# Kernel tuning notes

Measured on AMD Instinct MI355X. Metric: run time of the kernel, lower is better.

Reference implementation:

```python
import jax, jax.numpy as jnp
import numpy as np

L, D, H, FF, I, MAXREL = 6, 512, 8, 2048, 50, 128
HD = D // H
NREL = 2 * MAXREL + 1
EPS = 1e-5


def setup_inputs() -> dict:
    key = jax.random.key(0)
    ks = jax.random.split(key, 32)
    s = 0.02
    p = {
        'x': jax.random.normal(ks[0], (16, 512, I), dtype=jnp.float32),
        'in_w': jax.random.normal(ks[1], (I, D)) * s,
        'in_b': jnp.zeros((D,), jnp.float32),
        'Wq': jax.random.normal(ks[2], (L, D, D)) * s,
        'Wk': jax.random.normal(ks[3], (L, D, D)) * s,
        'Wv': jax.random.normal(ks[4], (L, D, D)) * s,
        'Wo': jax.random.normal(ks[5], (L, D, D)) * s,
        'bo': jnp.zeros((L, D), jnp.float32),
        'rel_emb': jax.random.normal(ks[6], (L, NREL, HD)) * s,
        'w1': jax.random.normal(ks[7], (L, D, FF)) * s,
        'b1': jnp.zeros((L, FF), jnp.float32),
        'w2': jax.random.normal(ks[8], (L, FF, D)) * s,
        'b2': jnp.zeros((L, D), jnp.float32),
        'ln1_g': jnp.ones((L, D), jnp.float32),
        'ln1_b': jnp.zeros((L, D), jnp.float32),
        'ln2_g': jnp.ones((L, D), jnp.float32),
        'ln2_b': jnp.zeros((L, D), jnp.float32),
        'on_g': jnp.ones((D,), jnp.float32),
        'on_b': jnp.zeros((D,), jnp.float32),
        'p1_w': jax.random.normal(ks[9], (D, D // 2)) * s,
        'p1_b': jnp.zeros((D // 2,), jnp.float32),
        'p2_w': jax.random.normal(ks[10], (D // 2, 1)) * s,
        'p2_b': jnp.zeros((1,), jnp.float32),
    }
    return p


def _layer_norm(x, g, b):
    m = jnp.mean(x, axis=-1, keepdims=True)
    v = jnp.mean(jnp.square(x - m), axis=-1, keepdims=True)
    return (x - m) * jax.lax.rsqrt(v + EPS) * g + b


def _sinusoidal_pe(seq_len, d_model):
    pos = jnp.arange(seq_len, dtype=jnp.float32)[:, None]
    div = jnp.exp(jnp.arange(0, d_model, 2, dtype=jnp.float32) * (-jnp.log(10000.0) / d_model))
    pe = jnp.zeros((seq_len, d_model), jnp.float32)
    pe = pe.at[:, 0::2].set(jnp.sin(pos * div))
    pe = pe.at[:, 1::2].set(jnp.cos(pos * div))
    return pe


def reference(x, in_w, in_b, Wq, Wk, Wv, Wo, bo, rel_emb, w1, b1, w2, b2,
              ln1_g, ln1_b, ln2_g, ln2_b, on_g, on_b, p1_w, p1_b, p2_w, p2_b):
    B, S, _ = x.shape
    scale = jnp.sqrt(jnp.float32(HD))
    # relative position index matrix [S, S] in [0, 2*MAXREL]
    r = jnp.arange(S)
    rel_idx = jnp.clip(r[None, :] - r[:, None], -MAXREL, MAXREL) + MAXREL

    h = x @ in_w + in_b                       # [B,S,D]
    h = h + _sinusoidal_pe(S, D)

    for l in range(L):
        q = (h @ Wq[l]).reshape(B, S, H, HD).transpose(0, 2, 1, 3)  # [B,H,S,hd]
        k = (h @ Wk[l]).reshape(B, S, H, HD).transpose(0, 2, 1, 3)
        v = (h @ Wv[l]).reshape(B, S, H, HD).transpose(0, 2, 1, 3)
        scores = jnp.einsum('bhqd,bhkd->bhqk', q, k) / scale
        rel = rel_emb[l][rel_idx]             # [S,S,hd]
        scores = scores + jnp.einsum('bhqd,qkd->bhqk', q, rel)  # rel bias is NOT scaled (matches source)
        attn = jax.nn.softmax(scores, axis=-1)
        ctx = jnp.einsum('bhqk,bhkd->bhqd', attn, v)
        ctx = ctx.transpose(0, 2, 1, 3).reshape(B, S, D)
        attn_out = ctx @ Wo[l] + bo[l]
        h = _layer_norm(h + attn_out, ln1_g[l], ln1_b[l])
        ff = jax.nn.relu(h @ w1[l] + b1[l]) @ w2[l] + b2[l]
        h = _layer_norm(h + ff, ln2_g[l], ln2_b[l])

    h = _layer_norm(h, on_g, on_b)
    out = jax.nn.relu(h @ p1_w + p1_b) @ p2_w + p2_b  # [B,S,1]
    return out
```

## Files before the change

### kernel.cpp

```cpp
#include <hip/hip_runtime.h>

typedef unsigned short u16;
typedef unsigned int   u32;
typedef short   short8  __attribute__((ext_vector_type(8)));
typedef float   floatx4 __attribute__((ext_vector_type(4)));
typedef int     intx4   __attribute__((ext_vector_type(4)));

#define NTOK 8192
#define SEQ  512
#define NLAYER 6

#define OFF_WT   ((size_t)0)
#define OFF_HB   ((size_t)38010880)
#define OFF_QKV  ((size_t)46399488)
#define OFF_CTX  ((size_t)71565312)
#define OFF_GOUT ((size_t)79953920)
#define OFF_FF   ((size_t)96731136)
#define OFF_HD1  ((size_t)130285568)
#define OFF_VT   OFF_FF
#define OFF_RELB OFF_HD1

#define LSTRIDE 3145728
#define P1T_OFF 18874368

__device__ __forceinline__ float b2f(u16 v) { return __uint_as_float(((u32)v) << 16); }
__device__ __forceinline__ float lo16(u32 v) { return __uint_as_float(v << 16); }
__device__ __forceinline__ float hi16(u32 v) { return __uint_as_float(v & 0xffff0000u); }
__device__ __forceinline__ u16 f2b(float f) {
  u32 x = __float_as_uint(f);
  return (u16)((x + 0x7fffu + ((x >> 16) & 1u)) >> 16);
}
__device__ __forceinline__ u32 pack2(float a, float b) {
  return (u32)f2b(a) | ((u32)f2b(b) << 16);
}
__device__ __forceinline__ u32 cvtpk(float a, float b) {
  u32 r;
  asm("v_cvt_pk_bf16_f32 %0, %1, %2" : "=v"(r) : "v"(a), "v"(b));
  return r;
}

typedef __attribute__((address_space(1))) void* gas_t;
typedef __attribute__((address_space(3))) void* las_t;

__global__ __launch_bounds__(256) void transpose_all(
    const float* __restrict__ Wq, const float* __restrict__ Wk,
    const float* __restrict__ Wv, const float* __restrict__ Wo,
    const float* __restrict__ w1, const float* __restrict__ w2,
    const float* __restrict__ p1, u16* __restrict__ wT)
{
  __shared__ u16 tile[64][65];
  const int tb = blockIdx.x;
  const float* src; u16* dst; int R, C, tidx;
  if (tb < 4608) {
    const int l = tb / 768, r = tb % 768;
    const size_t lofs = (size_t)l * LSTRIDE;
    if (r < 256) {
      const int m = r >> 6; tidx = r & 63; R = 512; C = 512;
      const float* bases[4] = {Wq, Wk, Wv, Wo};
      src = bases[m] + (size_t)l * 262144;
      dst = wT + lofs + (size_t)m * 262144;
    } else if (r < 512) {
      tidx = r - 256; R = 512; C = 2048;
      src = w1 + (size_t)l * 1048576; dst = wT + lofs + 1048576;
    } else {
      tidx = r - 512; R = 2048; C = 512;
      src = w2 + (size_t)l * 1048576; dst = wT + lofs + 2097152;
    }
  } else {
    tidx = tb - 4608; R = 512; C = 256;
    src = p1; dst = wT + P1T_OFF;
  }
  const int tcn = C >> 6;
  const int tr = tidx / tcn, tc = tidx % tcn;
  const int th = threadIdx.x;
  {
    const int lr = th >> 2, cg = (th & 3) * 16;
    const float* sp = src + (size_t)(tr*64 + lr) * C + tc*64 + cg;
    float4 f0 = *(const float4*)(sp);
    float4 f1 = *(const float4*)(sp + 4);
    float4 f2 = *(const float4*)(sp + 8);
    float4 f3 = *(const float4*)(sp + 12);
    u16* tp = &tile[lr][cg];
    tp[0]=f2b(f0.x); tp[1]=f2b(f0.y); tp[2]=f2b(f0.z); tp[3]=f2b(f0.w);
    tp[4]=f2b(f1.x); tp[5]=f2b(f1.y); tp[6]=f2b(f1.z); tp[7]=f2b(f1.w);
    tp[8]=f2b(f2.x); tp[9]=f2b(f2.y); tp[10]=f2b(f2.z); tp[11]=f2b(f2.w);
    tp[12]=f2b(f3.x); tp[13]=f2b(f3.y); tp[14]=f2b(f3.z); tp[15]=f2b(f3.w);
  }
  __syncthreads();
  {
    const int oc = th >> 2, rg = (th & 3) * 16;
    u32 wds[8];
    #pragma unroll
    for (int i = 0; i < 8; ++i)
      wds[i] = (u32)tile[rg + 2*i][oc] | ((u32)tile[rg + 2*i + 1][oc] << 16);
    u16* dp = dst + (size_t)(tc*64 + oc) * R + tr*64 + rg;
    uint4 o0; o0.x=wds[0]; o0.y=wds[1]; o0.z=wds[2]; o0.w=wds[3];
    uint4 o1; o1.x=wds[4]; o1.y=wds[5]; o1.z=wds[6]; o1.w=wds[7];
    *(uint4*)dp = o0;
    *(uint4*)(dp + 8) = o1;
  }
}

__global__ __launch_bounds__(128) void input_proj(
    const float* __restrict__ x, const float* __restrict__ w, const float* __restrict__ ib,
    u16* __restrict__ hb)
{
  const int row = blockIdx.x, t = threadIdx.x;
  const int s = row & (SEQ - 1);
  __shared__ float xs[50];
  if (t < 50) xs[t] = x[row*50 + t];
  __syncthreads();
  #pragma unroll
  for (int rep = 0; rep < 4; ++rep) {
    const int d = rep*128 + t;
    float acc = ib[d];
    #pragma unroll
    for (int i = 0; i < 50; ++i) acc += xs[i] * w[i*512 + d];
    const int ii = d >> 1;
    const float dv = __expf((float)(2*ii) * -0.017988946f);
    const float ang = (float)s * dv;
    const float pe = (d & 1) ? cosf(ang) : sinf(ang);
    hb[(size_t)row*512 + d] = f2b(acc + pe);
  }
}

__global__ __launch_bounds__(256) void gemm_bt(
    const u16* __restrict__ A, const u16* __restrict__ Bt,
    const float* __restrict__ bias,
    float* __restrict__ outF0, float* __restrict__ outF1, u16* __restrict__ outB,
    u16* __restrict__ vTout,
    const int M, const int N, const int K, const int kLen, const int flags)
{
  __shared__ __align__(16) u16 As[2*128*32];
  __shared__ __align__(16) u16 Bs[2*128*32];
  const int id = blockIdx.x;
  const int xcd = id & 7, rest = id >> 3;
  const int bm = (rest & 7) * 8 + xcd;
  const int bn = rest >> 3;
  const int z = blockIdx.y;
  const int kOff = z * kLen;
  const int m0 = bm << 7, n0 = bn << 7;
  const int tid = threadIdx.x;
  const int wave = tid >> 6, lane = tid & 63;
  const int wr = (wave >> 1) << 6, wc = (wave & 1) << 6;
  const int lrow = lane & 15, lquad = lane >> 4;

  floatx4 acc[4][4];
  #pragma unroll
  for (int i = 0; i < 4; ++i)
    #pragma unroll
    for (int j = 0; j < 4; ++j) { floatx4 zz = {0.f,0.f,0.f,0.f}; acc[i][j] = zz; }

  const u16* a0p = A  + (size_t)m0 * K + kOff;
  const u16* b0p = Bt + (size_t)n0 * K + kOff;
  const int c0 = tid, c1 = 256 + tid;
  const int ar0 = c0 >> 2, as0 = (c0 & 3) * 8;
  const int ar1 = c1 >> 2, as1 = (c1 & 3) * 8;

  for (int k0 = 0; k0 < kLen; k0 += 64) {
    #pragma unroll
    for (int hh = 0; hh < 2; ++hh) {
      const int kk = k0 + hh*32;
      __builtin_amdgcn_global_load_lds((gas_t)(a0p + (size_t)ar0*K + kk + as0), (las_t)(&As[hh*4096 + c0*8]), 16, 0, 0);
      __builtin_amdgcn_global_load_lds((gas_t)(a0p + (size_t)ar1*K + kk + as1), (las_t)(&As[hh*4096 + c1*8]), 16, 0, 0);
      __builtin_amdgcn_global_load_lds((gas_t)(b0p + (size_t)ar0*K + kk + as0), (las_t)(&Bs[hh*4096 + c0*8]), 16, 0, 0);
      __builtin_amdgcn_global_load_lds((gas_t)(b0p + (size_t)ar1*K + kk + as1), (las_t)(&Bs[hh*4096 + c1*8]), 16, 0, 0);
    }
    __syncthreads();
    #pragma unroll
    for (int hh = 0; hh < 2; ++hh) {
      short8 af[4], bf[4];
      #pragma unroll
      for (int i = 0; i < 4; ++i) af[i] = *(const short8*)&As[hh*4096 + (wr + i*16 + lrow)*32 + lquad*8];
      #pragma unroll
      for (int j = 0; j < 4; ++j) bf[j] = *(const short8*)&Bs[hh*4096 + (wc + j*16 + lrow)*32 + lquad*8];
      #pragma unroll
      for (int i = 0; i < 4; ++i)
        #pragma unroll
        for (int j = 0; j < 4; ++j)
          acc[i][j] = __builtin_amdgcn_mfma_f32_16x16x32_bf16(bf[j], af[i], acc[i][j], 0, 0, 0);
    }
    __syncthreads();
  }

  if ((flags & 4) && n0 >= 1024) {
    #pragma unroll
    for (int i = 0; i < 4; ++i) {
      const int row = m0 + wr + i*16 + lrow;
      const int bb = row >> 9, s = row & 511;
      #pragma unroll
      for (int j = 0; j < 4; ++j) {
        const int cm0 = (n0 - 1024) + wc + j*16 + lquad*4;
        #pragma unroll
        for (int v = 0; v < 4; ++v) {
          const int cm = cm0 + v;
          const int hh = cm >> 6, d = cm & 63;
          vTout[((size_t)(bb*8 + hh)*64 + d)*512 + s] = f2b(acc[i][j][v]);
        }
      }
    }
    return;
  }

  float* outF = (z == 0) ? outF0 : outF1;
  const bool hasb = ((flags & 1) != 0) && (z == 0);
  const bool dorelu = (flags & 2) != 0;
  #pragma unroll
  for (int i = 0; i < 4; ++i) {
    const int row = m0 + wr + i*16 + lrow;
    #pragma unroll
    for (int j = 0; j < 4; ++j) {
      const int colbase = n0 + wc + j*16 + lquad*4;
      float4 bv4 = make_float4(0.f, 0.f, 0.f, 0.f);
      if (hasb) bv4 = *(const float4*)(bias + colbase);
      float v0 = acc[i][j][0] + bv4.x;
      float v1 = acc[i][j][1] + bv4.y;
      float v2 = acc[i][j][2] + bv4.z;
      float v3 = acc[i][j][3] + bv4.w;
      if (dorelu) {
        v0 = fmaxf(v0, 0.f); v1 = fmaxf(v1, 0.f);
        v2 = fmaxf(v2, 0.f); v3 = fmaxf(v3, 0.f);
      }
      const size_t off = (size_t)row * N + colbase;
      if (outB) {
        uint2 o; o.x = pack2(v0, v1); o.y = pack2(v2, v3);
        *(uint2*)(outB + off) = o;
      } else {
        *(float4*)(outF + off) = make_float4(v0, v1, v2, v3);
      }
    }
  }
}

__global__ __launch_bounds__(256) void cvt_rel_all(
    const float* __restrict__ rel, u16* __restrict__ relB)
{
  const int i = blockIdx.x*256 + threadIdx.x;
  if (i < 6*257*64) {
    const int l = i / 16448, rem = i % 16448;
    relB[l*17408 + rem] = f2b(rel[i]);
  }
}

__global__ __launch_bounds__(256, 3) void attn_mfma(
    const u16* __restrict__ qkv, const u16* __restrict__ vT,
    const u16* __restrict__ relB, u16* __restrict__ ctx)
{
  const int id = blockIdx.x;
  const int xcd = id & 7, g = (id >> 3) & 15, qt = id >> 7;
  const int bh = xcd*16 + g;
  const int b = bh >> 3, h = bh & 7;
  const int t = threadIdx.x, w = t >> 6, lane = t & 63;
  const int lr = lane & 15, quad = lane >> 4;

  __shared__ __align__(16) u16 Ks[64*72];
  __shared__ __align__(16) u16 Vs[64*72];
  __shared__ __align__(16) u16 Pr[64*274];

  const size_t token0 = (size_t)b*512 + qt*64;
  const int srow = t >> 2, scol = (t & 3) * 16;
  const u16* kbase = qkv + (size_t)b*512*1536 + 512 + h*64;
  const u16* vbase = vT + (size_t)bh*64*512;

  short8 af0, af1;
  {
    const u16* qp = qkv + (token0 + w*16 + lr)*1536 + h*64 + quad*8;
    af0 = *(const short8*)(qp);
    af1 = *(const short8*)(qp + 32);
  }

  uint4 kr0, kr1, vr0, vr1;
  {
    const u16* kp = kbase + (size_t)srow*1536 + scol;
    kr0 = *(const uint4*)kp; kr1 = *(const uint4*)(kp + 8);
    const u16* vp = vbase + (size_t)srow*512 + scol;
    vr0 = *(const uint4*)vp; vr1 = *(const uint4*)(vp + 8);
  }

  #pragma unroll 4
  for (int nt = 0; nt < 17; ++nt) {
    const u16* rp = relB + (nt*16 + lr)*64 + quad*8;
    short8 rb0 = *(const short8*)(rp);
    short8 rb1 = *(const short8*)(rp + 32);
    floatx4 c = {0.f,0.f,0.f,0.f};
    c = __builtin_amdgcn_mfma_f32_16x16x32_bf16(af0, rb0, c, 0, 0, 0);
    c = __builtin_amdgcn_mfma_f32_16x16x32_bf16(af1, rb1, c, 0, 0, 0);
    #pragma unroll
    for (int r = 0; r < 4; ++r)
      Pr[(w*16 + quad*4 + r)*274 + nt*16 + lr] = f2b(c[r] * 1.44269504f);
  }

  floatx4 oacc[4];
  float lacc = 0.f;
  #pragma unroll
  for (int n = 0; n < 4; ++n) { floatx4 zz = {0.f,0.f,0.f,0.f}; oacc[n] = zz; }

  const int qglob = qt*64 + w*16 + lr;
  const int prbase = (w*16 + lr)*274 + 128;

  for (int kt = 0; kt < 8; ++kt) {
    __syncthreads();
    *(uint4*)&Ks[srow*72 + scol]     = kr0;
    *(uint4*)&Ks[srow*72 + scol + 8] = kr1;
    *(uint4*)&Vs[srow*72 + scol]     = vr0;
    *(uint4*)&Vs[srow*72 + scol + 8] = vr1;
    __syncthreads();

    if (kt < 7) {
      const u16* kp = kbase + (size_t)((kt+1)*64 + srow)*1536 + scol;
      kr0 = *(const uint4*)kp; kr1 = *(const uint4*)(kp + 8);
      const u16* vp = vbase + (size_t)srow*512 + (kt+1)*64 + scol;
      vr0 = *(const uint4*)vp; vr1 = *(const uint4*)(vp + 8);
    }

    floatx4 s4[4];
    __builtin_amdgcn_s_setprio(1);
    #pragma unroll
    for (int nt = 0; nt < 4; ++nt) {
      short8 kb0 = *(const short8*)&Ks[(nt*16 + lr)*72 + quad*8];
      short8 kb1 = *(const short8*)&Ks[(nt*16 + lr)*72 + 32 + quad*8];
      floatx4 c = {0.f,0.f,0.f,0.f};
      c = __builtin_amdgcn_mfma_f32_16x16x32_bf16(kb0, af0, c, 0, 0, 0);
      c = __builtin_amdgcn_mfma_f32_16x16x32_bf16(kb1, af1, c, 0, 0, 0);
      s4[nt] = c;
    }
    __builtin_amdgcn_s_setprio(0);

    u32 wq[4][2];
    const int kq = kt*64 + quad*4 - qglob;
    #pragma unroll
    for (int nt = 0; nt < 4; ++nt) {
      const int dbase = kq + nt*16;
      float p[4];
      #pragma unroll
      for (int r = 0; r < 4; ++r) {
        int dd = dbase + r;
        dd = dd < -128 ? -128 : (dd > 128 ? 128 : dd);
        p[r] = exp2f(fmaf(s4[nt][r], 0.18033688f, b2f(Pr[prbase + dd])));
      }
      lacc += (p[0] + p[1]) + (p[2] + p[3]);
      wq[nt][0] = cvtpk(p[0], p[1]);
      wq[nt][1] = cvtpk(p[2], p[3]);
    }

    intx4 pw0; pw0.x = (int)wq[0][0]; pw0.y = (int)wq[0][1];
               pw0.z = (int)wq[1][0]; pw0.w = (int)wq[1][1];
    intx4 pw1; pw1.x = (int)wq[2][0]; pw1.y = (int)wq[2][1];
               pw1.z = (int)wq[3][0]; pw1.w = (int)wq[3][1];
    const short8 pf0 = __builtin_bit_cast(short8, pw0);
    const short8 pf1 = __builtin_bit_cast(short8, pw1);

    __builtin_amdgcn_s_setprio(1);
    #pragma unroll
    for (int nd = 0; nd < 4; ++nd) {
      const int vrow = (nd*16 + lr)*72;
      uint2 a0 = *(const uint2*)&Vs[vrow + quad*4];
      uint2 a1 = *(const uint2*)&Vs[vrow + 16 + quad*4];
      uint2 a2 = *(const uint2*)&Vs[vrow + 32 + quad*4];
      uint2 a3 = *(const uint2*)&Vs[vrow + 48 + quad*4];
      intx4 v0; v0.x = (int)a0.x; v0.y = (int)a0.y; v0.z = (int)a1.x; v0.w = (int)a1.y;
      intx4 v1; v1.x = (int)a2.x; v1.y = (int)a2.y; v1.z = (int)a3.x; v1.w = (int)a3.y;
      const short8 vb0 = __builtin_bit_cast(short8, v0);
      const short8 vb1 = __builtin_bit_cast(short8, v1);
      oacc[nd] = __builtin_amdgcn_mfma_f32_16x16x32_bf16(vb0, pf0, oacc[nd], 0, 0, 0);
      oacc[nd] = __builtin_amdgcn_mfma_f32_16x16x32_bf16(vb1, pf1, oacc[nd], 0, 0, 0);
    }
    __builtin_amdgcn_s_setprio(0);
  }

  lacc += __shfl_xor(lacc, 16);
  lacc += __shfl_xor(lacc, 32);

  {
    const float inv = 1.f / lacc;
    u16* cp = ctx + (token0 + w*16 + lr)*512 + h*64;
    #pragma unroll
    for (int nd = 0; nd < 4; ++nd) {
      const int d = nd*16 + quad*4;
      uint2 o;
      o.x = pack2(oacc[nd][0]*inv, oacc[nd][1]*inv);
      o.y = pack2(oacc[nd][2]*inv, oacc[nd][3]*inv);
      *(uint2*)(cp + d) = o;
    }
  }
}

__global__ __launch_bounds__(128) void ln_kernel(
    const u16* __restrict__ resB, const float* __restrict__ add0,
    const float* __restrict__ add1,
    const float* __restrict__ g, const float* __restrict__ be,
    u16* __restrict__ hb)
{
  const int row = blockIdx.x, t = threadIdx.x;
  const size_t base = (size_t)row * 512;
  const u32 r0 = *(const u32*)(resB + base + t*4);
  const u32 r1 = *(const u32*)(resB + base + t*4 + 2);
  float x0 = lo16(r0), x1 = hi16(r0), x2 = lo16(r1), x3 = hi16(r1);
  if (add0) {
    const float4 a = *(const float4*)(add0 + base + t*4);
    x0 += a.x; x1 += a.y; x2 += a.z; x3 += a.w;
  }
  if (add1) {
    const float4 a = *(const float4*)(add1 + base + t*4);
    x0 += a.x; x1 += a.y; x2 += a.z; x3 += a.w;
  }
  float s = x0 + x1 + x2 + x3;
  #pragma unroll
  for (int off = 32; off > 0; off >>= 1) s += __shfl_down(s, off);
  __shared__ float red[2];
  const int wv = t >> 6, ln = t & 63;
  if (ln == 0) red[wv] = s;
  __syncthreads();
  const float mean = (red[0] + red[1]) * (1.f/512.f);
  const float dx0 = x0-mean, dx1 = x1-mean, dx2 = x2-mean, dx3 = x3-mean;
  float vs = dx0*dx0 + dx1*dx1 + dx2*dx2 + dx3*dx3;
  __syncthreads();
  #pragma unroll
  for (int off = 32; off > 0; off >>= 1) vs += __shfl_down(vs, off);
  if (ln == 0) red[wv] = vs;
  __syncthreads();
  const float var = (red[0] + red[1]) * (1.f/512.f);
  const float inv = 1.f / sqrtf(var + 1e-5f);
  const float4 gv = *(const float4*)(g + t*4);
  const float4 bv = *(const float4*)(be + t*4);
  const float y0 = dx0*inv*gv.x + bv.x;
  const float y1 = dx1*inv*gv.y + bv.y;
  const float y2 = dx2*inv*gv.z + bv.z;
  const float y3 = dx3*inv*gv.w + bv.w;
  u32* hp = (u32*)(hb + base + t*4);
  hp[0] = pack2(y0, y1); hp[1] = pack2(y2, y3);
}

__global__ __launch_bounds__(256) void head2_kernel(
    const u16* __restrict__ hd1, const float* __restrict__ p2w,
    const float* __restrict__ p2b, float* __restrict__ out)
{
  const int wv = threadIdx.x >> 6, ln = threadIdx.x & 63;
  const int row = blockIdx.x * 4 + wv;
  const u16* hp = hd1 + (size_t)row * 256 + ln*4;
  const u32 h0 = *(const u32*)hp, h1 = *(const u32*)(hp + 2);
  const float4 w = *(const float4*)(p2w + ln*4);
  float acc = lo16(h0)*w.x + hi16(h0)*w.y + lo16(h1)*w.z + hi16(h1)*w.w;
  #pragma unroll
  for (int off = 1; off < 64; off <<= 1) acc += __shfl_xor(acc, off);
  if (ln == 0) out[row] = acc + p2b[0];
}

extern "C" void kernel_launch(void* const* d_in, const int* in_sizes, int n_in,
                              void* d_out, int out_size, void* d_ws, size_t ws_size,
                              hipStream_t stream) {
  (void)in_sizes; (void)n_in; (void)out_size; (void)ws_size;
  const float* X    = (const float*)d_in[0];
  const float* INW  = (const float*)d_in[1];
  const float* INB  = (const float*)d_in[2];
  const float* WQ   = (const float*)d_in[3];
  const float* WK   = (const float*)d_in[4];
  const float* WV   = (const float*)d_in[5];
  const float* WO   = (const float*)d_in[6];
  const float* BO   = (const float*)d_in[7];
  const float* REL  = (const float*)d_in[8];
  const float* W1   = (const float*)d_in[9];
  const float* B1   = (const float*)d_in[10];
  const float* W2   = (const float*)d_in[11];
  const float* B2   = (const float*)d_in[12];
  const float* LN1G = (const float*)d_in[13];
  const float* LN1B = (const float*)d_in[14];
  const float* LN2G = (const float*)d_in[15];
  const float* LN2B = (const float*)d_in[16];
  const float* ONG  = (const float*)d_in[17];
  const float* ONB  = (const float*)d_in[18];
  const float* P1W  = (const float*)d_in[19];
  const float* P1B  = (const float*)d_in[20];
  const float* P2W  = (const float*)d_in[21];
  const float* P2B  = (const float*)d_in[22];
  float* out = (float*)d_out;

  char* ws = (char*)d_ws;
  u16*   wT    = (u16*)(ws + OFF_WT);
  u16*   hB    = (u16*)(ws + OFF_HB);
  u16*   qkv   = (u16*)(ws + OFF_QKV);
  u16*   ctx   = (u16*)(ws + OFF_CTX);
  float* gout0 = (float*)(ws + OFF_GOUT);
  float* gout1 = (float*)(ws + OFF_QKV);
  u16*   ff    = (u16*)(ws + OFF_FF);
  u16*   hd1   = (u16*)(ws + OFF_HD1);
  u16*   vTb   = (u16*)(ws + OFF_VT);
  u16*   relBa = (u16*)(ws + OFF_RELB);

  transpose_all<<<4640, 256, 0, stream>>>(WQ, WK, WV, WO, W1, W2, P1W, wT);
  cvt_rel_all<<<386, 256, 0, stream>>>(REL, relBa);
  input_proj<<<NTOK, 128, 0, stream>>>(X, INW, INB, hB);

  for (int l = 0; l < NLAYER; ++l) {
    const u16* wTl = wT + (size_t)l * LSTRIDE;
    gemm_bt<<<dim3(768,1), 256, 0, stream>>>(hB, wTl, nullptr, nullptr, nullptr, qkv, vTb,
                                             8192, 1536, 512, 512, 4);
    attn_mfma<<<1024, 256, 0, stream>>>(qkv, vTb, relBa + l*17408, ctx);
    gemm_bt<<<dim3(256,2), 256, 0, stream>>>(ctx, wTl + 786432, BO + l*512,
                                             gout0, gout1, nullptr, nullptr,
                                             8192, 512, 512, 256, 1);
    ln_kernel<<<NTOK, 128, 0, stream>>>(hB, gout0, gout1, LN1G + l*512, LN1B + l*512, hB);
    gemm_bt<<<dim3(1024,1), 256, 0, stream>>>(hB, wTl + 1048576, B1 + l*2048,
                                              nullptr, nullptr, ff, nullptr,
                                              8192, 2048, 512, 512, 3);
    gemm_bt<<<dim3(256,2), 256, 0, stream>>>(ff, wTl + 2097152, B2 + l*512,
                                             gout0, gout1, nullptr, nullptr,
                                             8192, 512, 2048, 1024, 1);
    ln_kernel<<<NTOK, 128, 0, stream>>>(hB, gout0, gout1, LN2G + l*512, LN2B + l*512, hB);
  }
  ln_kernel<<<NTOK, 128, 0, stream>>>(hB, nullptr, nullptr, ONG, ONB, hB);
  gemm_bt<<<dim3(128,1), 256, 0, stream>>>(hB, wT + P1T_OFF, P1B,
                                           nullptr, nullptr, hd1, nullptr,
                                           8192, 256, 512, 512, 3);
  head2_kernel<<<2048, 256, 0, stream>>>(hd1, P2W, P2B, out);
}
```

Measured before the change: 1.141 ms.

## Double-buffer GEMM LDS tiles and vectorize input projection

```diff
diff --git a/kernel.cpp b/kernel.cpp
--- a/kernel.cpp
+++ b/kernel.cpp
@@ -110,29 +110,38 @@
   __shared__ float xs[50];
   if (t < 50) xs[t] = x[row*50 + t];
   __syncthreads();
-  #pragma unroll
-  for (int rep = 0; rep < 4; ++rep) {
-    const int d = rep*128 + t;
-    float acc = ib[d];
-    #pragma unroll
-    for (int i = 0; i < 50; ++i) acc += xs[i] * w[i*512 + d];
-    const int ii = d >> 1;
-    const float dv = __expf((float)(2*ii) * -0.017988946f);
-    const float ang = (float)s * dv;
-    const float pe = (d & 1) ? cosf(ang) : sinf(ang);
-    hb[(size_t)row*512 + d] = f2b(acc + pe);
-  }
-}
-
-__global__ __launch_bounds__(256) void gemm_bt(
+  const int d0 = t * 4;
+  float4 acc = *(const float4*)(ib + d0);
+  #pragma unroll
+  for (int i = 0; i < 50; ++i) {
+    const float4 wv = *(const float4*)(w + i*512 + d0);
+    const float xv = xs[i];
+    acc.x = fmaf(xv, wv.x, acc.x);
+    acc.y = fmaf(xv, wv.y, acc.y);
+    acc.z = fmaf(xv, wv.z, acc.z);
+    acc.w = fmaf(xv, wv.w, acc.w);
+  }
+  const float cexp = -0.017988946f;
+  const float dv0 = __expf((float)d0 * cexp);
+  const float dv1 = __expf((float)(d0 + 2) * cexp);
+  float s0, c0, s1, c1;
+  __sincosf((float)s * dv0, &s0, &c0);
+  __sincosf((float)s * dv1, &s1, &c1);
+  acc.x += s0; acc.y += c0; acc.z += s1; acc.w += c1;
+  u32* hp = (u32*)(hb + (size_t)row*512 + d0);
+  hp[0] = pack2(acc.x, acc.y);
+  hp[1] = pack2(acc.z, acc.w);
+}
+
+__global__ __launch_bounds__(256, 2) void gemm_bt(
     const u16* __restrict__ A, const u16* __restrict__ Bt,
     const float* __restrict__ bias,
     float* __restrict__ outF0, float* __restrict__ outF1, u16* __restrict__ outB,
     u16* __restrict__ vTout,
     const int M, const int N, const int K, const int kLen, const int flags)
 {
-  __shared__ __align__(16) u16 As[2*128*32];
-  __shared__ __align__(16) u16 Bs[2*128*32];
+  __shared__ __align__(16) u16 As[2][8192];
+  __shared__ __align__(16) u16 Bs[2][8192];
   const int id = blockIdx.x;
   const int xcd = id & 7, rest = id >> 3;
   const int bm = (rest & 7) * 8 + xcd;
@@ -157,31 +166,48 @@
   const int ar0 = c0 >> 2, as0 = (c0 & 3) * 8;
   const int ar1 = c1 >> 2, as1 = (c1 & 3) * 8;
 
-  for (int k0 = 0; k0 < kLen; k0 += 64) {
-    #pragma unroll
-    for (int hh = 0; hh < 2; ++hh) {
-      const int kk = k0 + hh*32;
-      __builtin_amdgcn_global_load_lds((gas_t)(a0p + (size_t)ar0*K + kk + as0), (las_t)(&As[hh*4096 + c0*8]), 16, 0, 0);
-      __builtin_amdgcn_global_load_lds((gas_t)(a0p + (size_t)ar1*K + kk + as1), (las_t)(&As[hh*4096 + c1*8]), 16, 0, 0);
-      __builtin_amdgcn_global_load_lds((gas_t)(b0p + (size_t)ar0*K + kk + as0), (las_t)(&Bs[hh*4096 + c0*8]), 16, 0, 0);
-      __builtin_amdgcn_global_load_lds((gas_t)(b0p + (size_t)ar1*K + kk + as1), (las_t)(&Bs[hh*4096 + c1*8]), 16, 0, 0);
-    }
-    __syncthreads();
+#define STAGE_G(buf, k0) do {                                                                  \
+    __builtin_amdgcn_global_load_lds((gas_t)(a0p + (size_t)ar0*K + (k0) + as0),                \
+                                     (las_t)(&As[buf][c0*8]), 16, 0, 0);                       \
+    __builtin_amdgcn_global_load_lds((gas_t)(a0p + (size_t)ar1*K + (k0) + as1),                \
+                                     (las_t)(&As[buf][c1*8]), 16, 0, 0);                       \
+    __builtin_amdgcn_global_load_lds((gas_t)(b0p + (size_t)ar0*K + (k0) + as0),                \
+                                     (las_t)(&Bs[buf][c0*8]), 16, 0, 0);                       \
+    __builtin_amdgcn_global_load_lds((gas_t)(b0p + (size_t)ar1*K + (k0) + as1),                \
+                                     (las_t)(&Bs[buf][c1*8]), 16, 0, 0);                       \
+    __builtin_amdgcn_global_load_lds((gas_t)(a0p + (size_t)ar0*K + (k0) + 32 + as0),           \
+                                     (las_t)(&As[buf][4096 + c0*8]), 16, 0, 0);                \
+    __builtin_amdgcn_global_load_lds((gas_t)(a0p + (size_t)ar1*K + (k0) + 32 + as1),           \
+                                     (las_t)(&As[buf][4096 + c1*8]), 16, 0, 0);                \
+    __builtin_amdgcn_global_load_lds((gas_t)(b0p + (size_t)ar0*K + (k0) + 32 + as0),           \
+                                     (las_t)(&Bs[buf][4096 + c0*8]), 16, 0, 0);                \
+    __builtin_amdgcn_global_load_lds((gas_t)(b0p + (size_t)ar1*K + (k0) + 32 + as1),           \
+                                     (las_t)(&Bs[buf][4096 + c1*8]), 16, 0, 0);                \
+  } while (0)
+
+  const int nst = kLen >> 6;
+  STAGE_G(0, 0);
+  __syncthreads();
+
+  int cur = 0;
+  for (int t = 0; t < nst; ++t) {
+    if (t + 1 < nst) STAGE_G(cur ^ 1, (t + 1) * 64);
     #pragma unroll
     for (int hh = 0; hh < 2; ++hh) {
       short8 af[4], bf[4];
       #pragma unroll
-      for (int i = 0; i < 4; ++i) af[i] = *(const short8*)&As[hh*4096 + (wr + i*16 + lrow)*32 + lquad*8];
+      for (int i = 0; i < 4; ++i) af[i] = *(const short8*)&As[cur][hh*4096 + (wr + i*16 + lrow)*32 + lquad*8];
       #pragma unroll
-      for (int j = 0; j < 4; ++j) bf[j] = *(const short8*)&Bs[hh*4096 + (wc + j*16 + lrow)*32 + lquad*8];
+      for (int j = 0; j < 4; ++j) bf[j] = *(const short8*)&Bs[cur][hh*4096 + (wc + j*16 + lrow)*32 + lquad*8];
       #pragma unroll
       for (int i = 0; i < 4; ++i)
         #pragma unroll
         for (int j = 0; j < 4; ++j)
           acc[i][j] = __builtin_amdgcn_mfma_f32_16x16x32_bf16(bf[j], af[i], acc[i][j], 0, 0, 0);
     }
-    __syncthreads();
-  }
+    if (t + 1 < nst) { __syncthreads(); cur ^= 1; }
+  }
+#undef STAGE_G
 
   if ((flags & 4) && n0 >= 1024) {
     #pragma unroll
```

New measurement: 1.142 ms. Within noise of the previous version (+0.1%).
